# Performance work log

Measured on AMD Instinct MI355X. Metric: run time of the kernel, lower is better.

The kernel has to match this reference:

```python
import jax, jax.numpy as jnp
import numpy as np

N_NODES = 50000
N_GRAPHS = 64
NEG_SLOPE = 0.2


def gat_conv(x, src, dst, W, a_src, a_dst, b, n_nodes, concat):
    """PyG-style GATConv (eval mode, self-loops already in src/dst).
    x: [N, Fin], W: [Fin, H*C], a_src/a_dst: [H, C], b: [H*C] or [C].
    """
    H, C = a_src.shape
    h = (x @ W).reshape(n_nodes, H, C)                      # [N,H,C]
    al_src = jnp.einsum('nhc,hc->nh', h, a_src)             # [N,H]
    al_dst = jnp.einsum('nhc,hc->nh', h, a_dst)             # [N,H]
    e = jax.nn.leaky_relu(al_src[src] + al_dst[dst], NEG_SLOPE)  # [E,H]
    # softmax over incoming edges per destination node
    m = jax.ops.segment_max(e, dst, num_segments=n_nodes)   # [N,H]
    ex = jnp.exp(e - m[dst])
    s = jax.ops.segment_sum(ex, dst, num_segments=n_nodes)  # [N,H]
    alpha = ex / (s[dst] + 1e-16)                           # [E,H]
    # attention-weighted aggregation of source features
    out = jax.ops.segment_sum(h[src] * alpha[..., None], dst, num_segments=n_nodes)  # [N,H,C]
    out = out.reshape(n_nodes, H * C) if concat else out.mean(axis=1)
    return out + b


def setup_inputs() -> dict:
    key = jax.random.key(0)
    ks = jax.random.split(key, 12)
    n, e = N_NODES, 800000
    x = jax.random.normal(ks[0], (n, 500), dtype=jnp.float32)
    edge_index = jax.random.randint(ks[1], (2, e), 0, n, dtype=jnp.int64)
    batch = jnp.sort(jax.random.randint(ks[2], (n,), 0, N_GRAPHS, dtype=jnp.int64))
    hid, heads = 64, 4
    sc = 0.1
    W1 = jax.random.normal(ks[3], (500, heads * hid), dtype=jnp.float32) * sc
    a_src1 = jax.random.normal(ks[4], (heads, hid), dtype=jnp.float32) * sc
    a_dst1 = jax.random.normal(ks[5], (heads, hid), dtype=jnp.float32) * sc
    b1 = jnp.zeros((heads * hid,), dtype=jnp.float32)
    W2 = jax.random.normal(ks[6], (heads * hid, hid), dtype=jnp.float32) * sc
    a_src2 = jax.random.normal(ks[7], (1, hid), dtype=jnp.float32) * sc
    a_dst2 = jax.random.normal(ks[8], (1, hid), dtype=jnp.float32) * sc
    b2 = jnp.zeros((hid,), dtype=jnp.float32)
    Wl = jax.random.normal(ks[9], (hid, 2), dtype=jnp.float32) * sc
    bl = jnp.zeros((2,), dtype=jnp.float32)
    return dict(x=x, edge_index=edge_index, batch=batch,
                W1=W1, a_src1=a_src1, a_dst1=a_dst1, b1=b1,
                W2=W2, a_src2=a_src2, a_dst2=a_dst2, b2=b2,
                Wl=Wl, bl=bl)


def reference(x, edge_index, batch, W1, a_src1, a_dst1, b1,
              W2, a_src2, a_dst2, b2, Wl, bl):
    n = x.shape[0]
    # PyG GATConv adds self-loops by default
    loops = jnp.arange(n, dtype=edge_index.dtype)
    src = jnp.concatenate([edge_index[0], loops])
    dst = jnp.concatenate([edge_index[1], loops])
    h = jax.nn.relu(gat_conv(x, src, dst, W1, a_src1, a_dst1, b1, n, concat=True))
    h = jax.nn.relu(gat_conv(h, src, dst, W2, a_src2, a_dst2, b2, n, concat=False))
    # global mean pool over graphs
    sums = jax.ops.segment_sum(h, batch, num_segments=N_GRAPHS)      # [G, hid]
    cnt = jax.ops.segment_sum(jnp.ones((n,), h.dtype), batch, num_segments=N_GRAPHS)
    pooled = sums / jnp.maximum(cnt, 1.0)[:, None]
    return pooled @ Wl + bl                                          # [G, 2]
```

## Files before the change

kernel.cpp:

```cpp
#include <hip/hip_runtime.h>
#include <math.h>

#define NN   50000
#define NE   800000
#define NET  850000
#define NG   64
#define KIN  500
#define NEG  0.2f

typedef unsigned short ushort_t;
typedef __attribute__((ext_vector_type(8))) short bf8_t;
typedef __attribute__((ext_vector_type(8))) unsigned short us8_t;
typedef __attribute__((ext_vector_type(4))) float f4_t;
typedef __attribute__((ext_vector_type(2))) float f2_t;
typedef __attribute__((ext_vector_type(4))) unsigned u4_t;
typedef __attribute__((ext_vector_type(2))) unsigned u2_t;

__device__ __forceinline__ float bf2f(ushort_t u) {
    unsigned v = ((unsigned)u) << 16;
    return __builtin_bit_cast(float, v);
}
__device__ __forceinline__ ushort_t f2bf(float f) {
    unsigned b = __builtin_bit_cast(unsigned, f);
    unsigned r = (b + 0x7FFFu + ((b >> 16) & 1u)) >> 16;
    return (ushort_t)r;
}

#if __has_builtin(__builtin_amdgcn_cvt_f32_fp8)
#define FP8DEC(w, b) __builtin_amdgcn_cvt_f32_fp8((w), (b))
#else
__device__ __forceinline__ float fp8_sw_dec(unsigned w, int b) {
    unsigned by = (w >> (8 * b)) & 0xFFu;
    unsigned s = by >> 7, e = (by >> 3) & 15u, m = by & 7u;
    float v = e ? __builtin_bit_cast(float, ((e + 120u) << 23) | (m << 20))
                : (float)m * 0.001953125f;
    return s ? -v : v;
}
#define FP8DEC(w, b) fp8_sw_dec((w), (b))
#endif

#if __has_builtin(__builtin_amdgcn_cvt_pk_f32_fp8)
#define HAVE_PKDEC 1
__device__ __forceinline__ f2_t fp8_pk_lo(unsigned w) {
    return __builtin_amdgcn_cvt_pk_f32_fp8(w, false);
}
__device__ __forceinline__ f2_t fp8_pk_hi(unsigned w) {
    return __builtin_amdgcn_cvt_pk_f32_fp8(w, true);
}
#else
#define HAVE_PKDEC 0
__device__ __forceinline__ f2_t fp8_pk_lo(unsigned w) {
    f2_t r; r.x = FP8DEC(w, 0); r.y = FP8DEC(w, 1); return r;
}
__device__ __forceinline__ f2_t fp8_pk_hi(unsigned w) {
    f2_t r; r.x = FP8DEC(w, 2); r.y = FP8DEC(w, 3); return r;
}
#endif

#if __has_builtin(__builtin_amdgcn_cvt_pk_fp8_f32)
__device__ __forceinline__ unsigned char f2fp8(float f) {
    return (unsigned char)(__builtin_amdgcn_cvt_pk_fp8_f32(f, 0.f, 0u, false) & 0xFFu);
}
#else
__device__ __forceinline__ unsigned char f2fp8(float f) {
    unsigned u = __builtin_bit_cast(unsigned, f);
    unsigned sgn = (u >> 24) & 0x80u;
    float a = fabsf(f);
    if (!(a < 448.f)) return (unsigned char)(sgn | 0x7Eu);
    if (a < 0.015625f) {
        int m = (int)(a * 512.f + 0.5f);
        return (unsigned char)(sgn | (m > 7 ? 8 : m));
    }
    unsigned r = u + 0x7FFFFu + ((u >> 20) & 1u);
    unsigned e = (r >> 23) & 0xFFu;
    unsigned m = (r >> 20) & 7u;
    if (e > 135u) return (unsigned char)(sgn | 0x7Eu);
    return (unsigned char)(sgn | ((e - 120u) << 3) | m);
}
#endif

#define GLOAD_LDS(g, l)                                                        \
    __builtin_amdgcn_global_load_lds(                                          \
        (const __attribute__((address_space(1))) unsigned int*)(g),            \
        (__attribute__((address_space(3))) unsigned int*)(l), 16, 0, 0)

__global__ void k_deg(const int* __restrict__ ei, int* __restrict__ deg) {
    int e = blockIdx.x * 256 + threadIdx.x;
    if (e >= NET) return;
    int dst = (e < NE) ? ei[NE + e] : (e - NE);
    atomicAdd(&deg[dst], 1);
}

__global__ void k_scan_part(const int* __restrict__ deg, int* __restrict__ part) {
    __shared__ int s[256];
    int t = threadIdx.x;
    int i = blockIdx.x * 256 + t;
    s[t] = (i < NN) ? deg[i] : 0;
    __syncthreads();
    for (int off = 128; off > 0; off >>= 1) {
        if (t < off) s[t] += s[t + off];
        __syncthreads();
    }
    if (t == 0) part[blockIdx.x] = s[0];
}

__global__ void k_scan_top(int* __restrict__ part, int nb) {
    __shared__ int s[256];
    int t = threadIdx.x;
    int v = (t < nb) ? part[t] : 0;
    s[t] = v;
    __syncthreads();
    for (int off = 1; off < 256; off <<= 1) {
        int a = (t >= off) ? s[t - off] : 0;
        __syncthreads();
        s[t] += a;
        __syncthreads();
    }
    if (t < nb) part[t] = s[t] - v;
}

__global__ void k_scan_apply(const int* __restrict__ deg, const int* __restrict__ part,
                             int* __restrict__ rowptr) {
    __shared__ int s[256];
    int t = threadIdx.x;
    int i = blockIdx.x * 256 + t;
    int v = (i < NN) ? deg[i] : 0;
    s[t] = v;
    __syncthreads();
    for (int off = 1; off < 256; off <<= 1) {
        int a = (t >= off) ? s[t - off] : 0;
        __syncthreads();
        s[t] += a;
        __syncthreads();
    }
    if (i < NN) rowptr[i] = part[blockIdx.x] + s[t] - v;
    if (i == 0) rowptr[NN] = NET;
}

__global__ void k_fill(const int* __restrict__ ei, const int* __restrict__ rowptr,
                       int* __restrict__ cursor, int* __restrict__ csr) {
    int e = blockIdx.x * 256 + threadIdx.x;
    if (e >= NET) return;
    int src, dst;
    if (e < NE) { src = ei[e]; dst = ei[NE + e]; }
    else        { src = dst = e - NE; }
    int pos = atomicAdd(&cursor[dst], 1);
    csr[rowptr[dst] + pos] = src;
}

__global__ void k_cast_x(const float* __restrict__ x, ushort_t* __restrict__ xb) {
    int idx = blockIdx.x * 256 + threadIdx.x;
    if (idx >= 50048 * 128) return;
    int row = idx >> 7, k4 = (idx & 127) * 4;
    ushort4 o = make_ushort4(0, 0, 0, 0);
    if (row < NN && k4 < KIN) {
        float4 v = *(const float4*)&x[(size_t)row * KIN + k4];
        o.x = f2bf(v.x); o.y = f2bf(v.y); o.z = f2bf(v.z); o.w = f2bf(v.w);
    }
    *(ushort4*)&xb[(size_t)idx * 4] = o;
}

template <int KSRC, int KPAD, int NOUT>
__global__ void k_cast_wt(const float* __restrict__ W, ushort_t* __restrict__ Wt) {
    int idx = blockIdx.x * 256 + threadIdx.x;
    if (idx >= NOUT * KPAD) return;
    int n = idx / KPAD, k = idx - n * KPAD;
    float v = (k < KSRC) ? W[(size_t)k * NOUT + n] : 0.f;
    Wt[idx] = f2bf(v);
}

template <int K, int LDA, int BM, int BN, int WM, int FOUT, int HEADS>
__global__ __launch_bounds__(256) void k_mfma(
    const ushort_t* __restrict__ A, const ushort_t* __restrict__ Wt,
    const float* __restrict__ a_s, const float* __restrict__ a_d,
    unsigned char* __restrict__ Hb, float* __restrict__ als, float* __restrict__ ald)
{
    __shared__ __align__(16) ushort_t lA[BM * 32];
    __shared__ __align__(16) ushort_t lB[BN * 32];
    const int t    = threadIdx.x;
    const int row0 = blockIdx.y * BM;
    const int n0   = blockIdx.x * BN;
    const int ww   = t >> 6, lane = t & 63;
    const int wm   = ww % WM, wn = ww / WM;
    const int lrow = lane & 15, lq = lane >> 4;

    f4_t acc[4][4] = {};

    for (int k0 = 0; k0 < K; k0 += 32) {
#pragma unroll
        for (int i = 0; i < BM / 64; i++) {
            int c = i * 256 + t;
            int row = c >> 2, kq = c & 3;
            const ushort_t* gp = A + (size_t)(row0 + row) * LDA + k0 + kq * 8;
            GLOAD_LDS(gp, &lA[c * 8]);
        }
#pragma unroll
        for (int i = 0; i < BN / 64; i++) {
            int c = i * 256 + t;
            int row = c >> 2, kq = c & 3;
            const ushort_t* gp = Wt + (size_t)(n0 + row) * K + k0 + kq * 8;
            GLOAD_LDS(gp, &lB[c * 8]);
        }
        __syncthreads();
        bf8_t af[4], bfr[4];
#pragma unroll
        for (int i = 0; i < 4; i++)
            af[i] = *(const bf8_t*)&lA[(wm * 64 + i * 16 + lrow) * 32 + lq * 8];
#pragma unroll
        for (int j = 0; j < 4; j++)
            bfr[j] = *(const bf8_t*)&lB[(wn * 64 + j * 16 + lrow) * 32 + lq * 8];
#pragma unroll
        for (int i = 0; i < 4; i++)
#pragma unroll
            for (int j = 0; j < 4; j++)
                acc[i][j] = __builtin_amdgcn_mfma_f32_16x16x32_bf16(af[i], bfr[j], acc[i][j], 0, 0, 0);
        __syncthreads();
    }

    const int head = (n0 + wn * 64) >> 6;
    float as4[4], ad4[4];
#pragma unroll
    for (int j = 0; j < 4; j++) {
        as4[j] = a_s[head * 64 + j * 16 + lrow];
        ad4[j] = a_d[head * 64 + j * 16 + lrow];
    }
#pragma unroll
    for (int i = 0; i < 4; i++) {
#pragma unroll
        for (int r = 0; r < 4; r++) {
            int row = row0 + wm * 64 + i * 16 + lq * 4 + r;
            float v0 = acc[i][0][r], v1 = acc[i][1][r], v2 = acc[i][2][r], v3 = acc[i][3][r];
            if (row < NN) {
                size_t base = (size_t)row * FOUT + n0 + wn * 64 + lrow;
                Hb[base +  0] = f2fp8(v0);
                Hb[base + 16] = f2fp8(v1);
                Hb[base + 32] = f2fp8(v2);
                Hb[base + 48] = f2fp8(v3);
            }
            float ps = v0 * as4[0] + v1 * as4[1] + v2 * as4[2] + v3 * as4[3];
            float pd = v0 * ad4[0] + v1 * ad4[1] + v2 * ad4[2] + v3 * ad4[3];
#pragma unroll
            for (int off = 1; off < 16; off <<= 1) {
                ps += __shfl_xor(ps, off);
                pd += __shfl_xor(pd, off);
            }
            if (lrow == 0 && row < NN) {
                als[(size_t)row * HEADS + head] = ps;
                ald[(size_t)row * HEADS + head] = pd;
            }
        }
    }
}

#define CAP1 128
__global__ __launch_bounds__(256) void k_agg1(
    const int* __restrict__ rowptr, const int* __restrict__ csr,
    const unsigned char* __restrict__ Hb, const float* __restrict__ als,
    const float* __restrict__ ald, const float* __restrict__ bias,
    ushort_t* __restrict__ OutB)
{
    __shared__ float salpha[4][CAP1 * 4];
    int w = threadIdx.x >> 6, lane = threadIdx.x & 63;
    int dst = blockIdx.x * 4 + w;
    if (dst >= NN) return;
    float* Aw = salpha[w];
    const int beg = rowptr[dst], end = rowptr[dst + 1];
    const int deg = end - beg;

    const int hd    = lane & 3;
    const int slot  = lane >> 2;
    const int slot2 = lane >> 4;
    const int head2 = (lane >> 2) & 3;
    const int f0    = (lane & 3) * 16;

    int  ke    = slot2;
    bool valid = ke < deg;
    int  src   = csr[beg + (valid ? ke : 0)];
    u4_t xv    = *(const u4_t*)&Hb[(size_t)src * 256 + head2 * 64 + f0];

    const float adst = ald[dst * 4 + hd];
    float m = -1e30f, s = 0.f;
    for (int k = slot; k < deg; k += 16) {
        int sk = csr[beg + k];
        float e = als[sk * 4 + hd] + adst;
        e = (e > 0.f) ? e : NEG * e;
        if (k < CAP1) Aw[k * 4 + hd] = e;
        float mn = fmaxf(m, e);
        s = s * __expf(m - mn) + __expf(e - mn);
        m = mn;
    }
#pragma unroll
    for (int off = 4; off < 64; off <<= 1) {
        float mo = __shfl_xor(m, off);
        float so = __shfl_xor(s, off);
        float mn = fmaxf(m, mo);
        s = s * __expf(m - mn) + so * __expf(mo - mn);
        m = mn;
    }
    float inv = 1.f / (s + 1e-16f);
    int cap4 = (deg < CAP1 ? deg : CAP1) * 4;
    for (int j = lane; j < cap4; j += 64)
        Aw[j] = __expf(Aw[j] - m) * inv;

    const float m2  = __shfl(m, head2);
    const float i2  = __shfl(inv, head2);
    const float ad2 = __shfl(adst, head2);

    f2_t facc2[8] = {};
    int k0 = 0;
    while (true) {
        int k0n = k0 + 4;
        bool more = k0n < deg;
        int srcn = 0; u4_t xvn = {}; bool validn = false;
        if (more) {
            int ken = k0n + slot2;
            validn = ken < deg;
            srcn = csr[beg + (validn ? ken : 0)];
            xvn  = *(const u4_t*)&Hb[(size_t)srcn * 256 + head2 * 64 + f0];
        }
        float al = 0.f;
        if (valid) {
            if (ke < CAP1) {
                al = Aw[ke * 4 + head2];
            } else {
                float e = als[src * 4 + head2] + ad2;
                e = (e > 0.f) ? e : NEG * e;
                al = __expf(e - m2) * i2;
            }
        }
        f2_t al2; al2.x = al; al2.y = al;
#pragma unroll
        for (int wd = 0; wd < 4; wd++) {
            unsigned wv = xv[wd];
            facc2[wd * 2 + 0] += al2 * fp8_pk_lo(wv);
            facc2[wd * 2 + 1] += al2 * fp8_pk_hi(wv);
        }
        if (!more) break;
        k0 = k0n; ke = k0 + slot2; valid = validn; src = srcn; xv = xvn;
    }
    float facc[16];
#pragma unroll
    for (int j = 0; j < 8; j++) { facc[j * 2] = facc2[j].x; facc[j * 2 + 1] = facc2[j].y; }
#pragma unroll
    for (int j = 0; j < 16; j++) {
        facc[j] += __shfl_xor(facc[j], 16);
        facc[j] += __shfl_xor(facc[j], 32);
    }
    if (lane < 16) {
        us8_t oa, ob;
#pragma unroll
        for (int j = 0; j < 8; j++) {
            float o  = facc[j]     + bias[head2 * 64 + f0 + j];
            float o2 = facc[8 + j] + bias[head2 * 64 + f0 + 8 + j];
            oa[j] = f2bf(o  > 0.f ? o  : 0.f);
            ob[j] = f2bf(o2 > 0.f ? o2 : 0.f);
        }
        *(us8_t*)&OutB[(size_t)dst * 256 + head2 * 64 + f0]     = oa;
        *(us8_t*)&OutB[(size_t)dst * 256 + head2 * 64 + f0 + 8] = ob;
    }
}

#define CAP2 128
__global__ __launch_bounds__(256) void k_agg2(
    const int* __restrict__ rowptr, const int* __restrict__ csr,
    const unsigned char* __restrict__ Hb, const float* __restrict__ als,
    const float* __restrict__ ald, const float* __restrict__ bias,
    float* __restrict__ OutF)
{
    __shared__ float salpha2[4][CAP2];
    int w = threadIdx.x >> 6, lane = threadIdx.x & 63;
    int dst = blockIdx.x * 4 + w;
    if (dst >= NN) return;
    float* Aw = salpha2[w];
    const int beg = rowptr[dst], end = rowptr[dst + 1];
    const int deg = end - beg;
    const float adst = ald[dst];

    const int slot2 = lane >> 3;
    const int f0    = (lane & 7) * 8;

    int  ke    = slot2;
    bool valid = ke < deg;
    int  src   = csr[beg + (valid ? ke : 0)];
    u2_t xv    = *(const u2_t*)&Hb[(size_t)src * 64 + f0];

    float m = -1e30f, s = 0.f;
    for (int k = lane; k < deg; k += 64) {
        int sk = csr[beg + k];
        float e = als[sk] + adst;
        e = (e > 0.f) ? e : NEG * e;
        if (k < CAP2) Aw[k] = e;
        float mn = fmaxf(m, e);
        s = s * __expf(m - mn) + __expf(e - mn);
        m = mn;
    }
#pragma unroll
    for (int off = 1; off < 64; off <<= 1) {
        float mo = __shfl_xor(m, off);
        float so = __shfl_xor(s, off);
        float mn = fmaxf(m, mo);
        s = s * __expf(m - mn) + so * __expf(mo - mn);
        m = mn;
    }
    float inv = 1.f / (s + 1e-16f);
    int cap = deg < CAP2 ? deg : CAP2;
    for (int j = lane; j < cap; j += 64)
        Aw[j] = __expf(Aw[j] - m) * inv;

    f2_t facc2[4] = {};
    int k0 = 0;
    while (true) {
        int k0n = k0 + 8;
        bool more = k0n < deg;
        int srcn = 0; u2_t xvn = {}; bool validn = false;
        if (more) {
            int ken = k0n + slot2;
            validn = ken < deg;
            srcn = csr[beg + (validn ? ken : 0)];
            xvn  = *(const u2_t*)&Hb[(size_t)srcn * 64 + f0];
        }
        float al = 0.f;
        if (valid) {
            if (ke < CAP2) {
                al = Aw[ke];
            } else {
                float e = als[src] + adst;
                e = (e > 0.f) ? e : NEG * e;
                al = __expf(e - m) * inv;
            }
        }
        f2_t al2; al2.x = al; al2.y = al;
#pragma unroll
        for (int wd = 0; wd < 2; wd++) {
            unsigned wv = xv[wd];
            facc2[wd * 2 + 0] += al2 * fp8_pk_lo(wv);
            facc2[wd * 2 + 1] += al2 * fp8_pk_hi(wv);
        }
        if (!more) break;
        k0 = k0n; ke = k0 + slot2; valid = validn; src = srcn; xv = xvn;
    }
    float facc[8];
#pragma unroll
    for (int j = 0; j < 4; j++) { facc[j * 2] = facc2[j].x; facc[j * 2 + 1] = facc2[j].y; }
#pragma unroll
    for (int j = 0; j < 8; j++) {
        facc[j] += __shfl_xor(facc[j], 8);
        facc[j] += __shfl_xor(facc[j], 16);
        facc[j] += __shfl_xor(facc[j], 32);
    }
    if (lane < 8) {
        float4 oa, ob;
        float* pa = &oa.x; float* pb = &ob.x;
#pragma unroll
        for (int j = 0; j < 4; j++) {
            float v  = facc[j]     + bias[f0 + j];
            float v2 = facc[4 + j] + bias[f0 + 4 + j];
            pa[j] = (v  > 0.f) ? v  : 0.f;
            pb[j] = (v2 > 0.f) ? v2 : 0.f;
        }
        *(float4*)&OutF[(size_t)dst * 64 + f0]     = oa;
        *(float4*)&OutF[(size_t)dst * 64 + f0 + 4] = ob;
    }
}

#define PSPLIT 8
__global__ __launch_bounds__(256) void k_pool_part(
    const float* __restrict__ out2, const int* __restrict__ batch,
    float* __restrict__ pooled)
{
    int g = blockIdx.x >> 3, sp = blockIdx.x & 7;
    int lo, hi;
    { int a = 0, b = NN; while (a < b) { int mm = (a + b) >> 1; if (batch[mm] < g) a = mm + 1; else b = mm; } lo = a; }
    { int a = lo, b = NN; while (a < b) { int mm = (a + b) >> 1; if (batch[mm] < g + 1) a = mm + 1; else b = mm; } hi = a; }
    int t = threadIdx.x, c = t & 63, r = t >> 6;
    float s = 0.f;
    for (int n = lo + sp * 4 + r; n < hi; n += 32)
        s += out2[(size_t)n * 64 + c];
    __shared__ float red[256];
    red[t] = s;
    __syncthreads();
    if (t < 64) {
        float p = red[t] + red[t + 64] + red[t + 128] + red[t + 192];
        atomicAdd(&pooled[g * 64 + t], p);
    }
}

__global__ void k_final(const float* __restrict__ pooled, const int* __restrict__ batch,
                        const float* __restrict__ Wl, const float* __restrict__ bl,
                        float* __restrict__ out)
{
    int g = blockIdx.x;
    int lo, hi;
    { int a = 0, b = NN; while (a < b) { int mm = (a + b) >> 1; if (batch[mm] < g) a = mm + 1; else b = mm; } lo = a; }
    { int a = lo, b = NN; while (a < b) { int mm = (a + b) >> 1; if (batch[mm] < g + 1) a = mm + 1; else b = mm; } hi = a; }
    int t = threadIdx.x;
    int cnt = hi - lo;
    float p = pooled[g * 64 + t] / (float)(cnt > 0 ? cnt : 1);
    float r0 = p * Wl[t * 2 + 0];
    float r1 = p * Wl[t * 2 + 1];
#pragma unroll
    for (int off = 32; off > 0; off >>= 1) {
        r0 += __shfl_xor(r0, off);
        r1 += __shfl_xor(r1, off);
    }
    if (t == 0) {
        out[g * 2 + 0] = r0 + bl[0];
        out[g * 2 + 1] = r1 + bl[1];
    }
}

extern "C" void kernel_launch(void* const* d_in, const int* in_sizes, int n_in,
                              void* d_out, int out_size, void* d_ws, size_t ws_size,
                              hipStream_t stream)
{
    const float* x    = (const float*)d_in[0];
    const int*   ei   = (const int*)  d_in[1];
    const int*   batch= (const int*)  d_in[2];
    const float* W1   = (const float*)d_in[3];
    const float* as1  = (const float*)d_in[4];
    const float* ad1  = (const float*)d_in[5];
    const float* b1   = (const float*)d_in[6];
    const float* W2   = (const float*)d_in[7];
    const float* as2  = (const float*)d_in[8];
    const float* ad2  = (const float*)d_in[9];
    const float* b2   = (const float*)d_in[10];
    const float* Wl   = (const float*)d_in[11];
    const float* bl   = (const float*)d_in[12];
    float* out = (float*)d_out;

    int*   deg    = (int*)d_ws;
    int*   cursor = deg + 50048;
    int*   part   = cursor + 50048;
    int*   rowptr = part + 256;
    int*   csr    = rowptr + 50064;
    ushort_t* xb  = (ushort_t*)(csr + 850048);
    ushort_t* Wt1 = xb + (size_t)50048 * 512;
    ushort_t* Wt2 = Wt1 + 131072;
    ushort_t* h1b = Wt2 + 16384;
    unsigned char* h1b8 = (unsigned char*)h1b;
    float* al1s   = (float*)(h1b + (size_t)50000 * 256);
    float* al1d   = al1s + 200000;
    float* al2s   = al1d + 200000;
    float* al2d   = al2s + 50000;
    float* pooled = al2d + 50000;
    ushort_t* out1b = xb;
    unsigned char* h2b8 = (unsigned char*)(xb + 13000000);
    float*    out2  = (float*)(xb + 16400000);

    hipMemsetAsync(deg, 0, 2 * 50048 * sizeof(int), stream);
    hipMemsetAsync(pooled, 0, NG * 64 * sizeof(float), stream);

    k_deg       <<<(NET + 255) / 256, 256, 0, stream>>>(ei, deg);
    k_scan_part <<<196, 256, 0, stream>>>(deg, part);
    k_scan_top  <<<1,   256, 0, stream>>>(part, 196);
    k_scan_apply<<<196, 256, 0, stream>>>(deg, part, rowptr);
    k_fill      <<<(NET + 255) / 256, 256, 0, stream>>>(ei, rowptr, cursor, csr);

    k_cast_x<<<(50048 * 128 + 255) / 256, 256, 0, stream>>>(x, xb);
    k_cast_wt<500, 512, 256><<<(256 * 512 + 255) / 256, 256, 0, stream>>>(W1, Wt1);
    k_cast_wt<256, 256, 64> <<<(64 * 256 + 255) / 256, 256, 0, stream>>>(W2, Wt2);

    k_mfma<512, 512, 128, 128, 2, 256, 4><<<dim3(2, 391), 256, 0, stream>>>(
        xb, Wt1, as1, ad1, h1b8, al1s, al1d);
    k_agg1<<<(NN + 3) / 4, 256, 0, stream>>>(rowptr, csr, h1b8, al1s, al1d, b1, out1b);
    hipMemsetAsync(out1b + (size_t)50000 * 256, 0, (size_t)176 * 256 * sizeof(ushort_t), stream);

    k_mfma<256, 256, 256, 64, 4, 64, 1><<<dim3(1, 196), 256, 0, stream>>>(
        out1b, Wt2, as2, ad2, h2b8, al2s, al2d);
    k_agg2<<<(NN + 3) / 4, 256, 0, stream>>>(rowptr, csr, h2b8, al2s, al2d, b2, out2);

    k_pool_part<<<NG * PSPLIT, 256, 0, stream>>>(out2, batch, pooled);
    k_final    <<<NG, 64, 0, stream>>>(pooled, batch, Wl, bl, out);
}
```

Baseline: 425.8 us.

## Fuse fp32-to-bf16 cast of x into layer-1 MFMA GEMM with full-width tiles

Drops the separate kernel that cast x to a padded bf16 buffer. The first GEMM now reads fp32 x directly, converts it to bf16 in registers and writes it to LDS. The block grows to 512 threads covering all 256 output columns, so each x row is loaded once instead of once per column block. This removes a full write and re-read of the bf16 copy of x (about 50 MB), but the A tile no longer uses async global-to-LDS loads and the conversion now sits inside the GEMM loop.

```diff
diff --git a/kernel.cpp b/kernel.cpp
--- a/kernel.cpp
+++ b/kernel.cpp
@@ -40,7 +40,6 @@
 #endif
 
 #if __has_builtin(__builtin_amdgcn_cvt_pk_f32_fp8)
-#define HAVE_PKDEC 1
 __device__ __forceinline__ f2_t fp8_pk_lo(unsigned w) {
     return __builtin_amdgcn_cvt_pk_f32_fp8(w, false);
 }
@@ -48,7 +47,6 @@
     return __builtin_amdgcn_cvt_pk_f32_fp8(w, true);
 }
 #else
-#define HAVE_PKDEC 0
 __device__ __forceinline__ f2_t fp8_pk_lo(unsigned w) {
     f2_t r; r.x = FP8DEC(w, 0); r.y = FP8DEC(w, 1); return r;
 }
@@ -148,18 +146,6 @@
     csr[rowptr[dst] + pos] = src;
 }
 
-__global__ void k_cast_x(const float* __restrict__ x, ushort_t* __restrict__ xb) {
-    int idx = blockIdx.x * 256 + threadIdx.x;
-    if (idx >= 50048 * 128) return;
-    int row = idx >> 7, k4 = (idx & 127) * 4;
-    ushort4 o = make_ushort4(0, 0, 0, 0);
-    if (row < NN && k4 < KIN) {
-        float4 v = *(const float4*)&x[(size_t)row * KIN + k4];
-        o.x = f2bf(v.x); o.y = f2bf(v.y); o.z = f2bf(v.z); o.w = f2bf(v.w);
-    }
-    *(ushort4*)&xb[(size_t)idx * 4] = o;
-}
-
 template <int KSRC, int KPAD, int NOUT>
 __global__ void k_cast_wt(const float* __restrict__ W, ushort_t* __restrict__ Wt) {
     int idx = blockIdx.x * 256 + threadIdx.x;
@@ -167,6 +153,97 @@
     int n = idx / KPAD, k = idx - n * KPAD;
     float v = (k < KSRC) ? W[(size_t)k * NOUT + n] : 0.f;
     Wt[idx] = f2bf(v);
+}
+
+__global__ __launch_bounds__(512) void k_mfma1f(
+    const float* __restrict__ x, const ushort_t* __restrict__ Wt,
+    const float* __restrict__ a_s, const float* __restrict__ a_d,
+    unsigned char* __restrict__ Hb, float* __restrict__ als, float* __restrict__ ald)
+{
+    __shared__ __align__(16) ushort_t lA[128 * 32];
+    __shared__ __align__(16) ushort_t lB[256 * 32];
+    const int t    = threadIdx.x;
+    const int row0 = blockIdx.y * 128;
+    const int ww   = t >> 6, lane = t & 63;
+    const int wm   = ww & 1, wn = ww >> 1;
+    const int lrow = lane & 15, lq = lane >> 4;
+
+    const int arow  = t >> 2;
+    const int akq   = t & 3;
+    const int arowg = row0 + arow;
+    const bool arok = arowg < NN;
+    const float* xrow = x + (size_t)arowg * KIN;
+
+    f4_t acc[4][4] = {};
+
+    for (int k0 = 0; k0 < 512; k0 += 32) {
+        int kk = k0 + akq * 8;
+        float4 v0 = make_float4(0.f, 0.f, 0.f, 0.f);
+        float4 v1 = make_float4(0.f, 0.f, 0.f, 0.f);
+        if (arok && kk + 4 <= KIN) {
+            v0 = *(const float4*)(xrow + kk);
+            if (kk + 8 <= KIN) v1 = *(const float4*)(xrow + kk + 4);
+        }
+        us8_t ab;
+        ab[0] = f2bf(v0.x); ab[1] = f2bf(v0.y); ab[2] = f2bf(v0.z); ab[3] = f2bf(v0.w);
+        ab[4] = f2bf(v1.x); ab[5] = f2bf(v1.y); ab[6] = f2bf(v1.z); ab[7] = f2bf(v1.w);
+        *(us8_t*)&lA[arow * 32 + akq * 8] = ab;
+#pragma unroll
+        for (int i = 0; i < 2; i++) {
+            int c = i * 512 + t;
+            int row = c >> 2, kq = c & 3;
+            const ushort_t* gp = Wt + (size_t)row * 512 + k0 + kq * 8;
+            GLOAD_LDS(gp, &lB[c * 8]);
+        }
+        __syncthreads();
+        bf8_t af[4], bfr[4];
+#pragma unroll
+        for (int i = 0; i < 4; i++)
+            af[i] = *(const bf8_t*)&lA[(wm * 64 + i * 16 + lrow) * 32 + lq * 8];
+#pragma unroll
+        for (int j = 0; j < 4; j++)
+            bfr[j] = *(const bf8_t*)&lB[(wn * 64 + j * 16 + lrow) * 32 + lq * 8];
+#pragma unroll
+        for (int i = 0; i < 4; i++)
+#pragma unroll
+            for (int j = 0; j < 4; j++)
+                acc[i][j] = __builtin_amdgcn_mfma_f32_16x16x32_bf16(af[i], bfr[j], acc[i][j], 0, 0, 0);
+        __syncthreads();
+    }
+
+    const int head = wn;
+    float as4[4], ad4[4];
+#pragma unroll
+    for (int j = 0; j < 4; j++) {
+        as4[j] = a_s[head * 64 + j * 16 + lrow];
+        ad4[j] = a_d[head * 64 + j * 16 + lrow];
+    }
+#pragma unroll
+    for (int i = 0; i < 4; i++) {
+#pragma unroll
+        for (int r = 0; r < 4; r++) {
+            int row = row0 + wm * 64 + i * 16 + lq * 4 + r;
+            float v0 = acc[i][0][r], v1 = acc[i][1][r], v2 = acc[i][2][r], v3 = acc[i][3][r];
+            if (row < NN) {
+                size_t base = (size_t)row * 256 + wn * 64 + lrow;
+                Hb[base +  0] = f2fp8(v0);
+                Hb[base + 16] = f2fp8(v1);
+                Hb[base + 32] = f2fp8(v2);
+                Hb[base + 48] = f2fp8(v3);
+            }
+            float ps = v0 * as4[0] + v1 * as4[1] + v2 * as4[2] + v3 * as4[3];
+            float pd = v0 * ad4[0] + v1 * ad4[1] + v2 * ad4[2] + v3 * ad4[3];
+#pragma unroll
+            for (int off = 1; off < 16; off <<= 1) {
+                ps += __shfl_xor(ps, off);
+                pd += __shfl_xor(pd, off);
+            }
+            if (lrow == 0 && row < NN) {
+                als[(size_t)row * 4 + head] = ps;
+                ald[(size_t)row * 4 + head] = pd;
+            }
+        }
+    }
 }
 
 template <int K, int LDA, int BM, int BN, int WM, int FOUT, int HEADS>
@@ -556,12 +633,10 @@
     k_scan_apply<<<196, 256, 0, stream>>>(deg, part, rowptr);
     k_fill      <<<(NET + 255) / 256, 256, 0, stream>>>(ei, rowptr, cursor, csr);
 
-    k_cast_x<<<(50048 * 128 + 255) / 256, 256, 0, stream>>>(x, xb);
     k_cast_wt<500, 512, 256><<<(256 * 512 + 255) / 256, 256, 0, stream>>>(W1, Wt1);
     k_cast_wt<256, 256, 64> <<<(64 * 256 + 255) / 256, 256, 0, stream>>>(W2, Wt2);
 
-    k_mfma<512, 512, 128, 128, 2, 256, 4><<<dim3(2, 391), 256, 0, stream>>>(
-        xb, Wt1, as1, ad1, h1b8, al1s, al1d);
+    k_mfma1f<<<dim3(1, 391), 512, 0, stream>>>(x, Wt1, as1, ad1, h1b8, al1s, al1d);
     k_agg1<<<(NN + 3) / 4, 256, 0, stream>>>(rowptr, csr, h1b8, al1s, al1d, b1, out1b);
     hipMemsetAsync(out1b + (size_t)50000 * 256, 0, (size_t)176 * 256 * sizeof(ushort_t), stream);
 
```

New measurement: 419.0 us, median of 3. No clear change (-1.6%).
